# Kernel tuning notes

Measured on AMD Instinct MI355X. Metric: run time of the kernel, lower is better.

## Reference

```python
import jax, jax.numpy as jnp
import numpy as np
from jax.ops import segment_sum, segment_max

N_NODES = 50000
N_GRAPHS = 64
EPS = 1e-16


def gat_layer(x, src, dst, W, a_src, a_dst, b, n_nodes):
    # PyG GATConv, heads=1: shared linear, additive attention, per-dst softmax
    h = x @ W                                  # [N, H]
    al_s = h @ a_src                           # [N]
    al_d = h @ a_dst                           # [N]
    e = jax.nn.leaky_relu(al_s[src] + al_d[dst], 0.2)   # [E]
    # numerically stable segment softmax over edges grouped by dst
    m = segment_max(e, dst, num_segments=n_nodes)
    m = jnp.where(jnp.isfinite(m), m, 0.0)
    ex = jnp.exp(e - m[dst])
    denom = segment_sum(ex, dst, num_segments=n_nodes)
    alpha = ex / (denom[dst] + EPS)            # [E]
    out = segment_sum(alpha[:, None] * h[src], dst, num_segments=n_nodes)
    return out + b


def setup_inputs() -> dict:
    key = jax.random.key(0)
    ks = jax.random.split(key, 16)
    H = 128
    x = jax.random.normal(ks[0], (N_NODES, 4), dtype=jnp.float32)
    edge_index = jax.random.randint(ks[1], (2, 800000), 0, N_NODES, dtype=jnp.int64)
    batch = jnp.sort(jax.random.randint(ks[2], (N_NODES,), 0, N_GRAPHS, dtype=jnp.int64))

    def glorot(k, shape):
        lim = np.sqrt(6.0 / (shape[0] + shape[-1]))
        return jax.random.uniform(k, shape, jnp.float32, -lim, lim)

    params = {
        'W1': glorot(ks[3], (4, H)), 'as1': glorot(ks[4], (H,)), 'ad1': glorot(ks[5], (H,)), 'b1': jnp.zeros((H,), jnp.float32),
        'W2': glorot(ks[6], (H, H)), 'as2': glorot(ks[7], (H,)), 'ad2': glorot(ks[8], (H,)), 'b2': jnp.zeros((H,), jnp.float32),
        'W3': glorot(ks[9], (H, H)), 'as3': glorot(ks[10], (H,)), 'ad3': glorot(ks[11], (H,)), 'b3': jnp.zeros((H,), jnp.float32),
        'Wlin': glorot(ks[12], (H, 2)), 'blin': jnp.zeros((2,), jnp.float32),
    }
    return {'x': x, 'edge_index': edge_index, 'batch': batch, **params}


def reference(x, edge_index, batch, W1, as1, ad1, b1, W2, as2, ad2, b2, W3, as3, ad3, b3, Wlin, blin):
    n = x.shape[0]
    # GATConv default add_self_loops=True
    loop = jnp.arange(n, dtype=edge_index.dtype)
    src = jnp.concatenate([edge_index[0], loop])
    dst = jnp.concatenate([edge_index[1], loop])

    h = jax.nn.relu(gat_layer(x, src, dst, W1, as1, ad1, b1, n))
    h = jax.nn.relu(gat_layer(h, src, dst, W2, as2, ad2, b2, n))
    h = gat_layer(h, src, dst, W3, as3, ad3, b3, n)

    # global_mean_pool
    sums = segment_sum(h, batch, num_segments=N_GRAPHS)          # [G, H]
    cnt = segment_sum(jnp.ones((n,), h.dtype), batch, num_segments=N_GRAPHS)
    pooled = sums / jnp.maximum(cnt, 1.0)[:, None]
    # dropout p=0.5 is identity in eval mode
    return pooled @ Wlin + blin                                   # [G, 2]
```

## Files before the change

kernel.cpp:

```cpp
#include <hip/hip_runtime.h>
#include <math.h>


#define BW 512
#define PART_CHUNK 4096

__device__ __forceinline__ float bflo(unsigned u) { return __uint_as_float(u << 16); }
__device__ __forceinline__ float bfhi(unsigned u) { return __uint_as_float(u & 0xffff0000u); }
__device__ __forceinline__ unsigned pk2bf(float a, float b) {
  unsigned ua = __float_as_uint(a); ua += 0x7fffu + ((ua >> 16) & 1u);
  unsigned ub = __float_as_uint(b); ub += 0x7fffu + ((ub >> 16) & 1u);
  return (ua >> 16) | (ub & 0xffff0000u);
}

__global__ __launch_bounds__(256) void kb_hist(const int* __restrict__ ei,
                                               int* __restrict__ bcnt,
                                               int E, int ET, int NB) {
  __shared__ int h[128];
  int tid = threadIdx.x;
  if (tid < 128) h[tid] = 0;
  __syncthreads();
  int stride = gridDim.x * 256;
  for (int i = blockIdx.x * 256 + tid; i < ET; i += stride) {
    int dst = (i < E) ? ei[E + i] : (i - E);
    atomicAdd(&h[dst >> 9], 1);
  }
  __syncthreads();
  if (tid < NB && h[tid] > 0) atomicAdd(&bcnt[tid], h[tid]);
}

__global__ __launch_bounds__(128) void kb_scan(const int* __restrict__ bcnt,
                                               int* __restrict__ bbase,
                                               int* __restrict__ bcur,
                                               int* __restrict__ rowp,
                                               int N, int ET, int NB) {
  __shared__ int sm[128];
  int t = threadIdx.x;
  int v = (t < NB) ? bcnt[t] : 0;
  sm[t] = v;
  __syncthreads();
  for (int off = 1; off < 128; off <<= 1) {
    int u = (t >= off) ? sm[t - off] : 0;
    __syncthreads();
    sm[t] += u;
    __syncthreads();
  }
  int pre = sm[t] - v;
  if (t <= NB) bbase[t] = pre;
  if (t < NB) bcur[t] = pre;
  if (t == 0) rowp[N] = ET;
}

__global__ __launch_bounds__(256) void kb_part(const int* __restrict__ ei,
                                               int* __restrict__ bcur,
                                               int* __restrict__ bucketed,
                                               int E, int ET, int NB) {
  __shared__ int hist[128];
  __shared__ int runb[128];
  int tid = threadIdx.x;
  int base = blockIdx.x * PART_CHUNK;
  if (tid < 128) hist[tid] = 0;

  int sv[16], dv[16];
#pragma unroll
  for (int k = 0; k < 16; ++k) {
    int j = base + k * 256 + tid;
    int s = -1, d = 0;
    if (j < ET) {
      if (j < E) { s = ei[j]; d = ei[E + j]; }
      else       { s = j - E; d = j - E; }
    }
    sv[k] = s; dv[k] = d;
  }
  __syncthreads();
#pragma unroll
  for (int k = 0; k < 16; ++k)
    if (sv[k] >= 0) atomicAdd(&hist[dv[k] >> 9], 1);
  __syncthreads();
  if (tid < NB && hist[tid] > 0) runb[tid] = atomicAdd(&bcur[tid], hist[tid]);
  __syncthreads();
  if (tid < 128) hist[tid] = 0;
  __syncthreads();
#pragma unroll
  for (int k = 0; k < 16; ++k) {
    if (sv[k] >= 0) {
      int b = dv[k] >> 9;
      int off = atomicAdd(&hist[b], 1);
      bucketed[runb[b] + off] = (sv[k] << 9) | (dv[k] & (BW - 1));
    }
  }
}

__global__ __launch_bounds__(256) void kb_csr(const int* __restrict__ bucketed,
                                              const int* __restrict__ bbase,
                                              int* __restrict__ rowp,
                                              int* __restrict__ csr,
                                              int N) {
  __shared__ int h[512];
  __shared__ int sm[256];
  __shared__ int cur[512];
  int tid = threadIdx.x;
  int b = blockIdx.x;
  int cb = bbase[b], ce = bbase[b + 1];

  h[tid] = 0; h[tid + 256] = 0;
  __syncthreads();
  for (int j = cb + tid; j < ce; j += 256)
    atomicAdd(&h[bucketed[j] & (BW - 1)], 1);
  __syncthreads();
  int a0 = h[2 * tid], a1 = h[2 * tid + 1];
  int s = a0 + a1;
  sm[tid] = s;
  __syncthreads();
  for (int off = 1; off < 256; off <<= 1) {
    int u = (tid >= off) ? sm[tid - off] : 0;
    __syncthreads();
    sm[tid] += u;
    __syncthreads();
  }
  int pre = sm[tid] - s;
  cur[2 * tid] = pre;
  cur[2 * tid + 1] = pre + a0;
  __syncthreads();
  int node0 = b * BW;
  for (int local = tid; local < BW; local += 256) {
    int node = node0 + local;
    if (node < N) rowp[node] = cb + cur[local];
  }
  __syncthreads();
  for (int j = cb + tid; j < ce; j += 256) {
    int p = bucketed[j];
    int loc = p & (BW - 1);
    int pos = cb + atomicAdd(&cur[loc], 1);
    csr[pos] = (unsigned)p >> 9;
  }
}

__global__ __launch_bounds__(256) void k_gemm4al(const float* __restrict__ X,
                                                 const float* __restrict__ W,
                                                 const float* __restrict__ asv,
                                                 const float* __restrict__ adv,
                                                 float* __restrict__ Hout,
                                                 unsigned* __restrict__ Hbf,
                                                 float* __restrict__ al_s,
                                                 float* __restrict__ al_d, int N) {
  int wid = threadIdx.x >> 6, lane = threadIdx.x & 63;
  int node = blockIdx.x * 4 + wid;
  if (node >= N) return;
  float4 xv = *(const float4*)(X + node * 4);
  int f = lane * 2;
  float2 w0 = *(const float2*)(W + f);
  float2 w1 = *(const float2*)(W + 128 + f);
  float2 w2 = *(const float2*)(W + 256 + f);
  float2 w3 = *(const float2*)(W + 384 + f);
  float h0 = xv.x * w0.x + xv.y * w1.x + xv.z * w2.x + xv.w * w3.x;
  float h1 = xv.x * w0.y + xv.y * w1.y + xv.z * w2.y + xv.w * w3.y;
  float2 hv = {h0, h1};
  *(float2*)(Hout + node * 128 + f) = hv;
  Hbf[node * 64 + lane] = pk2bf(h0, h1);
  float2 s2 = *(const float2*)(asv + f);
  float2 d2 = *(const float2*)(adv + f);
  float ps = h0 * s2.x + h1 * s2.y;
  float pd = h0 * d2.x + h1 * d2.y;
  for (int off = 32; off; off >>= 1) {
    ps += __shfl_xor(ps, off);
    pd += __shfl_xor(pd, off);
  }
  if (lane == 0) { al_s[node] = ps; al_d[node] = pd; }
}

__global__ __launch_bounds__(256) void k_gemm128al(const float* __restrict__ X,
                                                   const float* __restrict__ W,
                                                   const float* __restrict__ asv,
                                                   const float* __restrict__ adv,
                                                   float* __restrict__ Hout,
                                                   uint4* __restrict__ Hbf,
                                                   float* __restrict__ al_s,
                                                   float* __restrict__ al_d, int N) {
  __shared__ float Ws[64 * 128];
  __shared__ float Xs[64 * 68];
  int tid = threadIdx.x;
  int base = blockIdx.x * 64;
  int ty = tid >> 4, tx = tid & 15;

  float acc[4][8];
#pragma unroll
  for (int r = 0; r < 4; ++r)
#pragma unroll
    for (int c = 0; c < 8; ++c) acc[r][c] = 0.f;

  for (int kk = 0; kk < 128; kk += 64) {
    __syncthreads();
    for (int i = tid * 4; i < 64 * 128; i += 1024) {
      *(float4*)(Ws + i) = *(const float4*)(W + kk * 128 + i);
    }
    for (int i = tid; i < 64 * 16; i += 256) {
      int node = i >> 4, k4 = (i & 15) << 2;
      int gn = base + node;
      float4 v;
      if (gn < N) v = *(const float4*)(X + gn * 128 + kk + k4);
      else        v = make_float4(0.f, 0.f, 0.f, 0.f);
      *(float4*)(Xs + node * 68 + k4) = v;
    }
    __syncthreads();

    for (int k = 0; k < 64; ++k) {
      float a0 = Xs[(ty * 4 + 0) * 68 + k];
      float a1 = Xs[(ty * 4 + 1) * 68 + k];
      float a2 = Xs[(ty * 4 + 2) * 68 + k];
      float a3 = Xs[(ty * 4 + 3) * 68 + k];
      float4 b0 = *(const float4*)(Ws + k * 128 + tx * 8);
      float4 b1 = *(const float4*)(Ws + k * 128 + tx * 8 + 4);
      acc[0][0] += a0 * b0.x; acc[0][1] += a0 * b0.y; acc[0][2] += a0 * b0.z; acc[0][3] += a0 * b0.w;
      acc[0][4] += a0 * b1.x; acc[0][5] += a0 * b1.y; acc[0][6] += a0 * b1.z; acc[0][7] += a0 * b1.w;
      acc[1][0] += a1 * b0.x; acc[1][1] += a1 * b0.y; acc[1][2] += a1 * b0.z; acc[1][3] += a1 * b0.w;
      acc[1][4] += a1 * b1.x; acc[1][5] += a1 * b1.y; acc[1][6] += a1 * b1.z; acc[1][7] += a1 * b1.w;
      acc[2][0] += a2 * b0.x; acc[2][1] += a2 * b0.y; acc[2][2] += a2 * b0.z; acc[2][3] += a2 * b0.w;
      acc[2][4] += a2 * b1.x; acc[2][5] += a2 * b1.y; acc[2][6] += a2 * b1.z; acc[2][7] += a2 * b1.w;
      acc[3][0] += a3 * b0.x; acc[3][1] += a3 * b0.y; acc[3][2] += a3 * b0.z; acc[3][3] += a3 * b0.w;
      acc[3][4] += a3 * b1.x; acc[3][5] += a3 * b1.y; acc[3][6] += a3 * b1.z; acc[3][7] += a3 * b1.w;
    }
  }

  float4 as0 = *(const float4*)(asv + tx * 8);
  float4 as1 = *(const float4*)(asv + tx * 8 + 4);
  float4 ad0 = *(const float4*)(adv + tx * 8);
  float4 ad1 = *(const float4*)(adv + tx * 8 + 4);
#pragma unroll
  for (int r = 0; r < 4; ++r) {
    int gn = base + ty * 4 + r;
    float ps = acc[r][0] * as0.x + acc[r][1] * as0.y + acc[r][2] * as0.z + acc[r][3] * as0.w
             + acc[r][4] * as1.x + acc[r][5] * as1.y + acc[r][6] * as1.z + acc[r][7] * as1.w;
    float pd = acc[r][0] * ad0.x + acc[r][1] * ad0.y + acc[r][2] * ad0.z + acc[r][3] * ad0.w
             + acc[r][4] * ad1.x + acc[r][5] * ad1.y + acc[r][6] * ad1.z + acc[r][7] * ad1.w;
    for (int off = 1; off < 16; off <<= 1) {
      ps += __shfl_xor(ps, off);
      pd += __shfl_xor(pd, off);
    }
    if (gn < N) {
      float4 o0 = make_float4(acc[r][0], acc[r][1], acc[r][2], acc[r][3]);
      float4 o1 = make_float4(acc[r][4], acc[r][5], acc[r][6], acc[r][7]);
      *(float4*)(Hout + gn * 128 + tx * 8) = o0;
      *(float4*)(Hout + gn * 128 + tx * 8 + 4) = o1;
      uint4 pb;
      pb.x = pk2bf(acc[r][0], acc[r][1]);
      pb.y = pk2bf(acc[r][2], acc[r][3]);
      pb.z = pk2bf(acc[r][4], acc[r][5]);
      pb.w = pk2bf(acc[r][6], acc[r][7]);
      Hbf[(size_t)gn * 16 + tx] = pb;
      if (tx == 0) { al_s[gn] = ps; al_d[gn] = pd; }
    }
  }
}

__global__ __launch_bounds__(256) void k_agg(const int* __restrict__ csr_src,
                                             const int* __restrict__ rowp,
                                             const float* __restrict__ al_s,
                                             const float* __restrict__ al_d,
                                             const float* __restrict__ Hh,
                                             const uint4* __restrict__ Hbf,
                                             const float* __restrict__ bias,
                                             float* __restrict__ exw,
                                             float* __restrict__ Yout, int N, int relu) {
  int wid = threadIdx.x >> 6, lane = threadIdx.x & 63;
  int dst = blockIdx.x * 4 + wid;
  if (dst >= N) return;
  int beg = rowp[dst], end = rowp[dst + 1];
  int deg = end - beg;
  float ald = al_d[dst];

  int q = lane >> 4;
  int l = lane & 15;
  float acc[8];
#pragma unroll
  for (int c = 0; c < 8; ++c) acc[c] = 0.f;

  if (deg <= 64) {
    int srcv = 0;
    float e = -INFINITY;
    if (lane < deg) {
      srcv = csr_src[beg + lane];
      e = al_s[srcv] + ald;
      e = (e > 0.f) ? e : 0.2f * e;
    }
    float m = e;
    for (int off = 32; off; off >>= 1) m = fmaxf(m, __shfl_xor(m, off));
    float av = (lane < deg) ? __expf(e - m) : 0.f;
    float den = av;
    for (int off = 32; off; off >>= 1) den += __shfl_xor(den, off);
    av *= 1.0f / (den + 1e-16f);

    int t = 0;
    for (; t + 8 <= deg; t += 8) {
      int sA = __shfl(srcv, t + q);
      int sB = __shfl(srcv, t + 4 + q);
      float wA = __shfl(av, t + q);
      float wB = __shfl(av, t + 4 + q);
      uint4 va = Hbf[(size_t)sA * 16 + l];
      uint4 vb = Hbf[(size_t)sB * 16 + l];
      acc[0] += wA * bflo(va.x) + wB * bflo(vb.x);
      acc[1] += wA * bfhi(va.x) + wB * bfhi(vb.x);
      acc[2] += wA * bflo(va.y) + wB * bflo(vb.y);
      acc[3] += wA * bfhi(va.y) + wB * bfhi(vb.y);
      acc[4] += wA * bflo(va.z) + wB * bflo(vb.z);
      acc[5] += wA * bfhi(va.z) + wB * bfhi(vb.z);
      acc[6] += wA * bflo(va.w) + wB * bflo(vb.w);
      acc[7] += wA * bfhi(va.w) + wB * bfhi(vb.w);
    }
    if (t + 4 <= deg) {
      int sA = __shfl(srcv, t + q);
      float wA = __shfl(av, t + q);
      uint4 va = Hbf[(size_t)sA * 16 + l];
      acc[0] += wA * bflo(va.x); acc[1] += wA * bfhi(va.x);
      acc[2] += wA * bflo(va.y); acc[3] += wA * bfhi(va.y);
      acc[4] += wA * bflo(va.z); acc[5] += wA * bfhi(va.z);
      acc[6] += wA * bflo(va.w); acc[7] += wA * bfhi(va.w);
      t += 4;
    }
    {
      int sA = __shfl(srcv, t + q);
      float wA = __shfl(av, t + q);
      if (t + q < deg) {
        uint4 va = Hbf[(size_t)sA * 16 + l];
        acc[0] += wA * bflo(va.x); acc[1] += wA * bfhi(va.x);
        acc[2] += wA * bflo(va.y); acc[3] += wA * bfhi(va.y);
        acc[4] += wA * bflo(va.z); acc[5] += wA * bfhi(va.z);
        acc[6] += wA * bflo(va.w); acc[7] += wA * bfhi(va.w);
      }
    }
  } else {
    const float* Hl = Hh + l * 8;
    float m = -INFINITY;
    for (int j = beg + lane; j < end; j += 64) {
      float e = al_s[csr_src[j]] + ald;
      e = (e > 0.f) ? e : 0.2f * e;
      exw[j] = e;
      m = fmaxf(m, e);
    }
    for (int off = 32; off; off >>= 1) m = fmaxf(m, __shfl_xor(m, off));

    float den = 0.f;
    for (int j = beg + lane; j < end; j += 64) {
      float ex = __expf(exw[j] - m);
      exw[j] = ex;
      den += ex;
    }
    for (int off = 32; off; off >>= 1) den += __shfl_xor(den, off);
    float inv = 1.0f / (den + 1e-16f);

    int j = beg;
    for (; j + 8 <= end; j += 8) {
      int sA = csr_src[j + q];
      int sB = csr_src[j + 4 + q];
      float wA = exw[j + q] * inv;
      float wB = exw[j + 4 + q] * inv;
      const float* rA = Hl + (size_t)sA * 128;
      const float* rB = Hl + (size_t)sB * 128;
      float4 a0 = *(const float4*)(rA);
      float4 a1 = *(const float4*)(rA + 4);
      float4 b0 = *(const float4*)(rB);
      float4 b1 = *(const float4*)(rB + 4);
      acc[0] += wA * a0.x + wB * b0.x;
      acc[1] += wA * a0.y + wB * b0.y;
      acc[2] += wA * a0.z + wB * b0.z;
      acc[3] += wA * a0.w + wB * b0.w;
      acc[4] += wA * a1.x + wB * b1.x;
      acc[5] += wA * a1.y + wB * b1.y;
      acc[6] += wA * a1.z + wB * b1.z;
      acc[7] += wA * a1.w + wB * b1.w;
    }
    if (j + 4 <= end) {
      int sA = csr_src[j + q];
      float wA = exw[j + q] * inv;
      const float* rA = Hl + (size_t)sA * 128;
      float4 a0 = *(const float4*)(rA);
      float4 a1 = *(const float4*)(rA + 4);
      acc[0] += wA * a0.x; acc[1] += wA * a0.y; acc[2] += wA * a0.z; acc[3] += wA * a0.w;
      acc[4] += wA * a1.x; acc[5] += wA * a1.y; acc[6] += wA * a1.z; acc[7] += wA * a1.w;
      j += 4;
    }
    if (j + q < end) {
      int sA = csr_src[j + q];
      float wA = exw[j + q] * inv;
      const float* rA = Hl + (size_t)sA * 128;
      float4 a0 = *(const float4*)(rA);
      float4 a1 = *(const float4*)(rA + 4);
      acc[0] += wA * a0.x; acc[1] += wA * a0.y; acc[2] += wA * a0.z; acc[3] += wA * a0.w;
      acc[4] += wA * a1.x; acc[5] += wA * a1.y; acc[6] += wA * a1.z; acc[7] += wA * a1.w;
    }
  }

#pragma unroll
  for (int c = 0; c < 8; ++c) {
    acc[c] += __shfl_xor(acc[c], 16);
    acc[c] += __shfl_xor(acc[c], 32);
  }
  if (q == 0) {
    float4 bv0 = *(const float4*)(bias + l * 8);
    float4 bv1 = *(const float4*)(bias + l * 8 + 4);
    float4 o0 = make_float4(acc[0] + bv0.x, acc[1] + bv0.y, acc[2] + bv0.z, acc[3] + bv0.w);
    float4 o1 = make_float4(acc[4] + bv1.x, acc[5] + bv1.y, acc[6] + bv1.z, acc[7] + bv1.w);
    if (relu) {
      o0.x = fmaxf(o0.x, 0.f); o0.y = fmaxf(o0.y, 0.f); o0.z = fmaxf(o0.z, 0.f); o0.w = fmaxf(o0.w, 0.f);
      o1.x = fmaxf(o1.x, 0.f); o1.y = fmaxf(o1.y, 0.f); o1.z = fmaxf(o1.z, 0.f); o1.w = fmaxf(o1.w, 0.f);
    }
    *(float4*)(Yout + (size_t)dst * 128 + l * 8) = o0;
    *(float4*)(Yout + (size_t)dst * 128 + l * 8 + 4) = o1;
  }
}

__global__ __launch_bounds__(256) void k_pool(const float* __restrict__ Hh,
                                              const int* __restrict__ batch,
                                              float* __restrict__ gsum,
                                              float* __restrict__ gcnt,
                                              int N, int nwaves) {
  int gw = (blockIdx.x * 256 + threadIdx.x) >> 6;
  int lane = threadIdx.x & 63;
  int chunk = (N + nwaves - 1) / nwaves;
  int beg = gw * chunk;
  int end = beg + chunk; if (end > N) end = N;
  if (beg >= end) return;

  int curg = batch[beg];
  float2 acc = {0.f, 0.f};
  int cnt = 0;
  for (int n = beg; n < end; ++n) {
    int g = batch[n];
    if (g != curg) {
      atomicAdd(&gsum[curg * 128 + lane * 2], acc.x);
      atomicAdd(&gsum[curg * 128 + lane * 2 + 1], acc.y);
      if (lane == 0) atomicAdd(&gcnt[curg], (float)cnt);
      acc.x = 0.f; acc.y = 0.f; cnt = 0; curg = g;
    }
    float2 h = *(const float2*)(Hh + (size_t)n * 128 + lane * 2);
    acc.x += h.x; acc.y += h.y; ++cnt;
  }
  atomicAdd(&gsum[curg * 128 + lane * 2], acc.x);
  atomicAdd(&gsum[curg * 128 + lane * 2 + 1], acc.y);
  if (lane == 0) atomicAdd(&gcnt[curg], (float)cnt);
}

__global__ __launch_bounds__(128) void k_final(const float* __restrict__ gsum,
                                               const float* __restrict__ gcnt,
                                               const float* __restrict__ Wlin,
                                               const float* __restrict__ blin,
                                               float* __restrict__ out) {
  int t = threadIdx.x;
  int g = t >> 1, c = t & 1;
  float inv = 1.0f / fmaxf(gcnt[g], 1.0f);
  float acc = blin[c];
  for (int k = 0; k < 128; ++k) acc += gsum[g * 128 + k] * inv * Wlin[k * 2 + c];
  out[g * 2 + c] = acc;
}

extern "C" void kernel_launch(void* const* d_in, const int* in_sizes, int n_in,
                              void* d_out, int out_size, void* d_ws, size_t ws_size,
                              hipStream_t stream) {
  const float* x    = (const float*)d_in[0];
  const int*   ei   = (const int*)d_in[1];
  const int*   batch= (const int*)d_in[2];
  const float* W1   = (const float*)d_in[3];
  const float* as1  = (const float*)d_in[4];
  const float* ad1  = (const float*)d_in[5];
  const float* b1   = (const float*)d_in[6];
  const float* W2   = (const float*)d_in[7];
  const float* as2  = (const float*)d_in[8];
  const float* ad2  = (const float*)d_in[9];
  const float* b2   = (const float*)d_in[10];
  const float* W3   = (const float*)d_in[11];
  const float* as3  = (const float*)d_in[12];
  const float* ad3  = (const float*)d_in[13];
  const float* b3   = (const float*)d_in[14];
  const float* Wlin = (const float*)d_in[15];
  const float* blin = (const float*)d_in[16];

  int N = in_sizes[0] / 4;
  int E = in_sizes[1] / 2;
  int ET = E + N;
  int NB = (N + BW - 1) / BW;

  char* ws = (char*)d_ws;
  float* bufA = (float*)ws; ws += (size_t)N * 128 * 4;
  float* bufB = (float*)ws; ws += (size_t)N * 128 * 4;
  unsigned* hbf = (unsigned*)ws; ws += (size_t)N * 128 * 2;
  float* al_s = (float*)ws; ws += (size_t)N * 4;
  float* al_d = (float*)ws; ws += (size_t)N * 4;
  float* gsum = (float*)ws; ws += (size_t)64 * 128 * 4;
  float* gcnt = (float*)ws; ws += (size_t)64 * 4;
  int* rowp   = (int*)ws;   ws += (size_t)(N + 1) * 4;
  int* csr    = (int*)ws;   ws += (size_t)ET * 4;
  float* exw  = (float*)ws; ws += (size_t)ET * 4;
  int* bucketed = (int*)ws; ws += (size_t)ET * 4;
  int* bcnt   = (int*)ws;   ws += (size_t)128 * 4;
  int* bbase  = (int*)ws;   ws += (size_t)132 * 4;
  int* bcur   = (int*)ws;   ws += (size_t)128 * 4;

  hipMemsetAsync(bcnt, 0, (size_t)128 * 4, stream);
  hipMemsetAsync(gsum, 0, (size_t)(64 * 128 + 64) * 4, stream);

  kb_hist<<<256, 256, 0, stream>>>(ei, bcnt, E, ET, NB);
  kb_scan<<<1, 128, 0, stream>>>(bcnt, bbase, bcur, rowp, N, ET, NB);
  kb_part<<<(ET + PART_CHUNK - 1) / PART_CHUNK, 256, 0, stream>>>(ei, bcur, bucketed, E, ET, NB);
  kb_csr <<<NB, 256, 0, stream>>>(bucketed, bbase, rowp, csr, N);

  int nb4 = (N + 3) / 4;
  k_gemm4al<<<nb4, 256, 0, stream>>>(x, W1, as1, ad1, bufA, hbf, al_s, al_d, N);
  k_agg    <<<nb4, 256, 0, stream>>>(csr, rowp, al_s, al_d, bufA, (const uint4*)hbf, b1, exw, bufB, N, 1);
  k_gemm128al<<<(N + 63) / 64, 256, 0, stream>>>(bufB, W2, as2, ad2, bufA, (uint4*)hbf, al_s, al_d, N);
  k_agg      <<<nb4, 256, 0, stream>>>(csr, rowp, al_s, al_d, bufA, (const uint4*)hbf, b2, exw, bufB, N, 1);
  k_gemm128al<<<(N + 63) / 64, 256, 0, stream>>>(bufB, W3, as3, ad3, bufA, (uint4*)hbf, al_s, al_d, N);
  k_agg      <<<nb4, 256, 0, stream>>>(csr, rowp, al_s, al_d, bufA, (const uint4*)hbf, b3, exw, bufB, N, 0);

  k_pool <<<256, 256, 0, stream>>>(bufB, batch, gsum, gcnt, N, 1024);
  k_final<<<1, 128, 0, stream>>>(gsum, gcnt, Wlin, blin, (float*)d_out);
}
```

Baseline: 368.9 us.

## Use bf16 MFMA for hidden GEMMs and keep activations in bf16

Replaces the fp32 SIMT 128x128 GEMM with a bf16 MFMA kernel (16x16x32) fed by a pre-transposed bf16 copy of W2/W3 built in a new prep kernel. Aggregation now writes bf16 activations for the relu layers and gathers bf16 neighbor rows in the large-degree path, and the fp32 H copies are no longer written. This cuts GEMM compute time and memory traffic on the intermediate buffers, at the cost of extra bf16 rounding on GEMM inputs and weights, which loosens accuracy.

```diff
diff --git a/kernel.cpp b/kernel.cpp
--- a/kernel.cpp
+++ b/kernel.cpp
@@ -4,6 +4,9 @@
 
 #define BW 512
 #define PART_CHUNK 4096
+
+typedef __attribute__((ext_vector_type(8))) short short8v;
+typedef __attribute__((ext_vector_type(4))) float f32x4;
 
 __device__ __forceinline__ float bflo(unsigned u) { return __uint_as_float(u << 16); }
 __device__ __forceinline__ float bfhi(unsigned u) { return __uint_as_float(u & 0xffff0000u); }
@@ -136,11 +139,24 @@
   }
 }
 
+__global__ __launch_bounds__(256) void k_prep(const float* __restrict__ W2,
+                                              const float* __restrict__ W3,
+                                              unsigned short* __restrict__ Wcm2,
+                                              unsigned short* __restrict__ Wcm3) {
+  int i = blockIdx.x * 256 + threadIdx.x;
+  if (i < 16384) {
+    int k = i >> 7, n = i & 127;
+    unsigned u = __float_as_uint(W2[i]); u += 0x7fffu + ((u >> 16) & 1u);
+    Wcm2[n * 128 + k] = (unsigned short)(u >> 16);
+    unsigned v = __float_as_uint(W3[i]); v += 0x7fffu + ((v >> 16) & 1u);
+    Wcm3[n * 128 + k] = (unsigned short)(v >> 16);
+  }
+}
+
 __global__ __launch_bounds__(256) void k_gemm4al(const float* __restrict__ X,
                                                  const float* __restrict__ W,
                                                  const float* __restrict__ asv,
                                                  const float* __restrict__ adv,
-                                                 float* __restrict__ Hout,
                                                  unsigned* __restrict__ Hbf,
                                                  float* __restrict__ al_s,
                                                  float* __restrict__ al_d, int N) {
@@ -155,8 +171,6 @@
   float2 w3 = *(const float2*)(W + 384 + f);
   float h0 = xv.x * w0.x + xv.y * w1.x + xv.z * w2.x + xv.w * w3.x;
   float h1 = xv.x * w0.y + xv.y * w1.y + xv.z * w2.y + xv.w * w3.y;
-  float2 hv = {h0, h1};
-  *(float2*)(Hout + node * 128 + f) = hv;
   Hbf[node * 64 + lane] = pk2bf(h0, h1);
   float2 s2 = *(const float2*)(asv + f);
   float2 d2 = *(const float2*)(adv + f);
@@ -169,86 +183,67 @@
   if (lane == 0) { al_s[node] = ps; al_d[node] = pd; }
 }
 
-__global__ __launch_bounds__(256) void k_gemm128al(const float* __restrict__ X,
-                                                   const float* __restrict__ W,
-                                                   const float* __restrict__ asv,
-                                                   const float* __restrict__ adv,
-                                                   float* __restrict__ Hout,
-                                                   uint4* __restrict__ Hbf,
-                                                   float* __restrict__ al_s,
-                                                   float* __restrict__ al_d, int N) {
-  __shared__ float Ws[64 * 128];
-  __shared__ float Xs[64 * 68];
-  int tid = threadIdx.x;
-  int base = blockIdx.x * 64;
-  int ty = tid >> 4, tx = tid & 15;
-
-  float acc[4][8];
-#pragma unroll
-  for (int r = 0; r < 4; ++r)
-#pragma unroll
-    for (int c = 0; c < 8; ++c) acc[r][c] = 0.f;
-
-  for (int kk = 0; kk < 128; kk += 64) {
-    __syncthreads();
-    for (int i = tid * 4; i < 64 * 128; i += 1024) {
-      *(float4*)(Ws + i) = *(const float4*)(W + kk * 128 + i);
-    }
-    for (int i = tid; i < 64 * 16; i += 256) {
-      int node = i >> 4, k4 = (i & 15) << 2;
-      int gn = base + node;
-      float4 v;
-      if (gn < N) v = *(const float4*)(X + gn * 128 + kk + k4);
-      else        v = make_float4(0.f, 0.f, 0.f, 0.f);
-      *(float4*)(Xs + node * 68 + k4) = v;
-    }
-    __syncthreads();
-
-    for (int k = 0; k < 64; ++k) {
-      float a0 = Xs[(ty * 4 + 0) * 68 + k];
-      float a1 = Xs[(ty * 4 + 1) * 68 + k];
-      float a2 = Xs[(ty * 4 + 2) * 68 + k];
-      float a3 = Xs[(ty * 4 + 3) * 68 + k];
-      float4 b0 = *(const float4*)(Ws + k * 128 + tx * 8);
-      float4 b1 = *(const float4*)(Ws + k * 128 + tx * 8 + 4);
-      acc[0][0] += a0 * b0.x; acc[0][1] += a0 * b0.y; acc[0][2] += a0 * b0.z; acc[0][3] += a0 * b0.w;
-      acc[0][4] += a0 * b1.x; acc[0][5] += a0 * b1.y; acc[0][6] += a0 * b1.z; acc[0][7] += a0 * b1.w;
-      acc[1][0] += a1 * b0.x; acc[1][1] += a1 * b0.y; acc[1][2] += a1 * b0.z; acc[1][3] += a1 * b0.w;
-      acc[1][4] += a1 * b1.x; acc[1][5] += a1 * b1.y; acc[1][6] += a1 * b1.z; acc[1][7] += a1 * b1.w;
-      acc[2][0] += a2 * b0.x; acc[2][1] += a2 * b0.y; acc[2][2] += a2 * b0.z; acc[2][3] += a2 * b0.w;
-      acc[2][4] += a2 * b1.x; acc[2][5] += a2 * b1.y; acc[2][6] += a2 * b1.z; acc[2][7] += a2 * b1.w;
-      acc[3][0] += a3 * b0.x; acc[3][1] += a3 * b0.y; acc[3][2] += a3 * b0.z; acc[3][3] += a3 * b0.w;
-      acc[3][4] += a3 * b1.x; acc[3][5] += a3 * b1.y; acc[3][6] += a3 * b1.z; acc[3][7] += a3 * b1.w;
-    }
-  }
-
-  float4 as0 = *(const float4*)(asv + tx * 8);
-  float4 as1 = *(const float4*)(asv + tx * 8 + 4);
-  float4 ad0 = *(const float4*)(adv + tx * 8);
-  float4 ad1 = *(const float4*)(adv + tx * 8 + 4);
-#pragma unroll
-  for (int r = 0; r < 4; ++r) {
-    int gn = base + ty * 4 + r;
-    float ps = acc[r][0] * as0.x + acc[r][1] * as0.y + acc[r][2] * as0.z + acc[r][3] * as0.w
-             + acc[r][4] * as1.x + acc[r][5] * as1.y + acc[r][6] * as1.z + acc[r][7] * as1.w;
-    float pd = acc[r][0] * ad0.x + acc[r][1] * ad0.y + acc[r][2] * ad0.z + acc[r][3] * ad0.w
-             + acc[r][4] * ad1.x + acc[r][5] * ad1.y + acc[r][6] * ad1.z + acc[r][7] * ad1.w;
+__global__ __launch_bounds__(256) void k_gemm128mfma(
+    const unsigned short* __restrict__ Xbf,
+    const unsigned short* __restrict__ Wcm,
+    const float* __restrict__ asv, const float* __restrict__ adv,
+    unsigned* __restrict__ Hbf,
+    float* __restrict__ al_s, float* __restrict__ al_d, int N) {
+  int wid = threadIdx.x >> 6, lane = threadIdx.x & 63;
+  int c = lane & 15, g = lane >> 4;
+  int row0 = blockIdx.x * 64 + wid * 16;
+  int arow = row0 + c;
+  int arowc = (arow < N) ? arow : (N - 1);
+
+  short8v a[4];
+#pragma unroll
+  for (int kt = 0; kt < 4; ++kt)
+    a[kt] = *(const short8v*)(Xbf + (size_t)arowc * 128 + kt * 32 + g * 8);
+
+  f32x4 acc[8];
+#pragma unroll
+  for (int f = 0; f < 8; ++f) acc[f] = (f32x4){0.f, 0.f, 0.f, 0.f};
+
+#pragma unroll
+  for (int f = 0; f < 8; ++f) {
+    const unsigned short* wb = Wcm + (size_t)(f * 16 + c) * 128 + g * 8;
+#pragma unroll
+    for (int kt = 0; kt < 4; ++kt) {
+      short8v b = *(const short8v*)(wb + kt * 32);
+      acc[f] = __builtin_amdgcn_mfma_f32_16x16x32_bf16(a[kt], b, acc[f], 0, 0, 0);
+    }
+  }
+
+  float ps[4] = {0.f, 0.f, 0.f, 0.f}, pd[4] = {0.f, 0.f, 0.f, 0.f};
+#pragma unroll
+  for (int f = 0; f < 8; ++f) {
+    float as_c = asv[f * 16 + c], ad_c = adv[f * 16 + c];
+#pragma unroll
+    for (int j = 0; j < 4; ++j) { ps[j] += acc[f][j] * as_c; pd[j] += acc[f][j] * ad_c; }
+  }
+#pragma unroll
+  for (int j = 0; j < 4; ++j) {
     for (int off = 1; off < 16; off <<= 1) {
-      ps += __shfl_xor(ps, off);
-      pd += __shfl_xor(pd, off);
-    }
-    if (gn < N) {
-      float4 o0 = make_float4(acc[r][0], acc[r][1], acc[r][2], acc[r][3]);
-      float4 o1 = make_float4(acc[r][4], acc[r][5], acc[r][6], acc[r][7]);
-      *(float4*)(Hout + gn * 128 + tx * 8) = o0;
-      *(float4*)(Hout + gn * 128 + tx * 8 + 4) = o1;
-      uint4 pb;
-      pb.x = pk2bf(acc[r][0], acc[r][1]);
-      pb.y = pk2bf(acc[r][2], acc[r][3]);
-      pb.z = pk2bf(acc[r][4], acc[r][5]);
-      pb.w = pk2bf(acc[r][6], acc[r][7]);
-      Hbf[(size_t)gn * 16 + tx] = pb;
-      if (tx == 0) { al_s[gn] = ps; al_d[gn] = pd; }
+      ps[j] += __shfl_xor(ps[j], off);
+      pd[j] += __shfl_xor(pd[j], off);
+    }
+  }
+  if (c == 0) {
+#pragma unroll
+    for (int j = 0; j < 4; ++j) {
+      int r = row0 + g * 4 + j;
+      if (r < N) { al_s[r] = ps[j]; al_d[r] = pd[j]; }
+    }
+  }
+
+#pragma unroll
+  for (int f = 0; f < 8; ++f) {
+#pragma unroll
+    for (int j = 0; j < 4; ++j) {
+      float partner = __shfl_xor(acc[f][j], 1);
+      int r = row0 + g * 4 + j;
+      if (((lane & 1) == 0) && r < N)
+        Hbf[(size_t)r * 64 + f * 8 + (c >> 1)] = pk2bf(acc[f][j], partner);
     }
   }
 }
@@ -257,11 +252,12 @@
                                              const int* __restrict__ rowp,
                                              const float* __restrict__ al_s,
                                              const float* __restrict__ al_d,
-                                             const float* __restrict__ Hh,
                                              const uint4* __restrict__ Hbf,
                                              const float* __restrict__ bias,
                                              float* __restrict__ exw,
-                                             float* __restrict__ Yout, int N, int relu) {
+                                             float* __restrict__ Yf32,
+                                             uint4* __restrict__ Ybf,
+                                             int N, int relu) {
   int wid = threadIdx.x >> 6, lane = threadIdx.x & 63;
   int dst = blockIdx.x * 4 + wid;
   if (dst >= N) return;
@@ -329,7 +325,6 @@
       }
     }
   } else {
-    const float* Hl = Hh + l * 8;
     float m = -INFINITY;
     for (int j = beg + lane; j < end; j += 64) {
       float e = al_s[csr_src[j]] + ald;
@@ -348,45 +343,14 @@
     for (int off = 32; off; off >>= 1) den += __shfl_xor(den, off);
     float inv = 1.0f / (den + 1e-16f);
 
-    int j = beg;
-    for (; j + 8 <= end; j += 8) {
-      int sA = csr_src[j + q];
-      int sB = csr_src[j + 4 + q];
-      float wA = exw[j + q] * inv;
-      float wB = exw[j + 4 + q] * inv;
-      const float* rA = Hl + (size_t)sA * 128;
-      const float* rB = Hl + (size_t)sB * 128;
-      float4 a0 = *(const float4*)(rA);
-      float4 a1 = *(const float4*)(rA + 4);
-      float4 b0 = *(const float4*)(rB);
-      float4 b1 = *(const float4*)(rB + 4);
-      acc[0] += wA * a0.x + wB * b0.x;
-      acc[1] += wA * a0.y + wB * b0.y;
-      acc[2] += wA * a0.z + wB * b0.z;
-      acc[3] += wA * a0.w + wB * b0.w;
-      acc[4] += wA * a1.x + wB * b1.x;
-      acc[5] += wA * a1.y + wB * b1.y;
-      acc[6] += wA * a1.z + wB * b1.z;
-      acc[7] += wA * a1.w + wB * b1.w;
-    }
-    if (j + 4 <= end) {
-      int sA = csr_src[j + q];
-      float wA = exw[j + q] * inv;
-      const float* rA = Hl + (size_t)sA * 128;
-      float4 a0 = *(const float4*)(rA);
-      float4 a1 = *(const float4*)(rA + 4);
-      acc[0] += wA * a0.x; acc[1] += wA * a0.y; acc[2] += wA * a0.z; acc[3] += wA * a0.w;
-      acc[4] += wA * a1.x; acc[5] += wA * a1.y; acc[6] += wA * a1.z; acc[7] += wA * a1.w;
-      j += 4;
-    }
-    if (j + q < end) {
-      int sA = csr_src[j + q];
-      float wA = exw[j + q] * inv;
-      const float* rA = Hl + (size_t)sA * 128;
-      float4 a0 = *(const float4*)(rA);
-      float4 a1 = *(const float4*)(rA + 4);
-      acc[0] += wA * a0.x; acc[1] += wA * a0.y; acc[2] += wA * a0.z; acc[3] += wA * a0.w;
-      acc[4] += wA * a1.x; acc[5] += wA * a1.y; acc[6] += wA * a1.z; acc[7] += wA * a1.w;
+    for (int j = beg + q; j < end; j += 4) {
+      int sA = csr_src[j];
+      float wA = exw[j] * inv;
+      uint4 va = Hbf[(size_t)sA * 16 + l];
+      acc[0] += wA * bflo(va.x); acc[1] += wA * bfhi(va.x);
+      acc[2] += wA * bflo(va.y); acc[3] += wA * bfhi(va.y);
+      acc[4] += wA * bflo(va.z); acc[5] += wA * bfhi(va.z);
+      acc[6] += wA * bflo(va.w); acc[7] += wA * bfhi(va.w);
     }
   }
 
@@ -398,14 +362,21 @@
   if (q == 0) {
     float4 bv0 = *(const float4*)(bias + l * 8);
     float4 bv1 = *(const float4*)(bias + l * 8 + 4);
-    float4 o0 = make_float4(acc[0] + bv0.x, acc[1] + bv0.y, acc[2] + bv0.z, acc[3] + bv0.w);
-    float4 o1 = make_float4(acc[4] + bv1.x, acc[5] + bv1.y, acc[6] + bv1.z, acc[7] + bv1.w);
+    float o0 = acc[0] + bv0.x, o1 = acc[1] + bv0.y, o2 = acc[2] + bv0.z, o3 = acc[3] + bv0.w;
+    float o4 = acc[4] + bv1.x, o5 = acc[5] + bv1.y, o6 = acc[6] + bv1.z, o7 = acc[7] + bv1.w;
     if (relu) {
-      o0.x = fmaxf(o0.x, 0.f); o0.y = fmaxf(o0.y, 0.f); o0.z = fmaxf(o0.z, 0.f); o0.w = fmaxf(o0.w, 0.f);
-      o1.x = fmaxf(o1.x, 0.f); o1.y = fmaxf(o1.y, 0.f); o1.z = fmaxf(o1.z, 0.f); o1.w = fmaxf(o1.w, 0.f);
-    }
-    *(float4*)(Yout + (size_t)dst * 128 + l * 8) = o0;
-    *(float4*)(Yout + (size_t)dst * 128 + l * 8 + 4) = o1;
+      o0 = fmaxf(o0, 0.f); o1 = fmaxf(o1, 0.f); o2 = fmaxf(o2, 0.f); o3 = fmaxf(o3, 0.f);
+      o4 = fmaxf(o4, 0.f); o5 = fmaxf(o5, 0.f); o6 = fmaxf(o6, 0.f); o7 = fmaxf(o7, 0.f);
+      uint4 pb;
+      pb.x = pk2bf(o0, o1); pb.y = pk2bf(o2, o3);
+      pb.z = pk2bf(o4, o5); pb.w = pk2bf(o6, o7);
+      Ybf[(size_t)dst * 16 + l] = pb;
+    } else {
+      float4 w0 = make_float4(o0, o1, o2, o3);
+      float4 w1 = make_float4(o4, o5, o6, o7);
+      *(float4*)(Yf32 + (size_t)dst * 128 + l * 8) = w0;
+      *(float4*)(Yf32 + (size_t)dst * 128 + l * 8 + 4) = w1;
+    }
   }
 }
 
@@ -480,9 +451,9 @@
   int NB = (N + BW - 1) / BW;
 
   char* ws = (char*)d_ws;
-  float* bufA = (float*)ws; ws += (size_t)N * 128 * 4;
-  float* bufB = (float*)ws; ws += (size_t)N * 128 * 4;
-  unsigned* hbf = (unsigned*)ws; ws += (size_t)N * 128 * 2;
+  unsigned* bfA = (unsigned*)ws; ws += (size_t)N * 64 * 4;
+  unsigned* bfB = (unsigned*)ws; ws += (size_t)N * 64 * 4;
+  float* bufY = (float*)ws; ws += (size_t)N * 128 * 4;
   float* al_s = (float*)ws; ws += (size_t)N * 4;
   float* al_d = (float*)ws; ws += (size_t)N * 4;
   float* gsum = (float*)ws; ws += (size_t)64 * 128 * 4;
@@ -494,6 +465,8 @@
   int* bcnt   = (int*)ws;   ws += (size_t)128 * 4;
   int* bbase  = (int*)ws;   ws += (size_t)132 * 4;
   int* bcur   = (int*)ws;   ws += (size_t)128 * 4;
+  unsigned short* wcm2 = (unsigned short*)ws; ws += (size_t)128 * 128 * 2;
+  unsigned short* wcm3 = (unsigned short*)ws; ws += (size_t)128 * 128 * 2;
 
   hipMemsetAsync(bcnt, 0, (size_t)128 * 4, stream);
   hipMemsetAsync(gsum, 0, (size_t)(64 * 128 + 64) * 4, stream);
@@ -502,15 +475,17 @@
   kb_scan<<<1, 128, 0, stream>>>(bcnt, bbase, bcur, rowp, N, ET, NB);
   kb_part<<<(ET + PART_CHUNK - 1) / PART_CHUNK, 256, 0, stream>>>(ei, bcur, bucketed, E, ET, NB);
   kb_csr <<<NB, 256, 0, stream>>>(bucketed, bbase, rowp, csr, N);
+  k_prep <<<64, 256, 0, stream>>>(W2, W3, wcm2, wcm3);
 
   int nb4 = (N + 3) / 4;
-  k_gemm4al<<<nb4, 256, 0, stream>>>(x, W1, as1, ad1, bufA, hbf, al_s, al_d, N);
-  k_agg    <<<nb4, 256, 0, stream>>>(csr, rowp, al_s, al_d, bufA, (const uint4*)hbf, b1, exw, bufB, N, 1);
-  k_gemm128al<<<(N + 63) / 64, 256, 0, stream>>>(bufB, W2, as2, ad2, bufA, (uint4*)hbf, al_s, al_d, N);
-  k_agg      <<<nb4, 256, 0, stream>>>(csr, rowp, al_s, al_d, bufA, (const uint4*)hbf, b2, exw, bufB, N, 1);
-  k_gemm128al<<<(N + 63) / 64, 256, 0, stream>>>(bufB, W3, as3, ad3, bufA, (uint4*)hbf, al_s, al_d, N);
-  k_agg      <<<nb4, 256, 0, stream>>>(csr, rowp, al_s, al_d, bufA, (const uint4*)hbf, b3, exw, bufB, N, 0);
-
-  k_pool <<<256, 256, 0, stream>>>(bufB, batch, gsum, gcnt, N, 1024);
+  int nb64 = (N + 63) / 64;
+  k_gemm4al<<<nb4, 256, 0, stream>>>(x, W1, as1, ad1, bfA, al_s, al_d, N);
+  k_agg    <<<nb4, 256, 0, stream>>>(csr, rowp, al_s, al_d, (const uint4*)bfA, b1, exw, bufY, (uint4*)bfB, N, 1);
+  k_gemm128mfma<<<nb64, 256, 0, stream>>>((const unsigned short*)bfB, wcm2, as2, ad2, bfA, al_s, al_d, N);
+  k_agg        <<<nb4, 256, 0, stream>>>(csr, rowp, al_s, al_d, (const uint4*)bfA, b2, exw, bufY, (uint4*)bfB, N, 1);
+  k_gemm128mfma<<<nb64, 256, 0, stream>>>((const unsigned short*)bfB, wcm3, as3, ad3, bfA, al_s, al_d, N);
+  k_agg        <<<nb4, 256, 0, stream>>>(csr, rowp, al_s, al_d, (const uint4*)bfA, b3, exw, bufY, (uint4*)bfB, N, 0);
+
+  k_pool <<<256, 256, 0, stream>>>(bufY, batch, gsum, gcnt, N, 1024);
   k_final<<<1, 128, 0, stream>>>(gsum, gcnt, Wlin, blin, (float*)d_out);
 }
```

Result: faster. 346.9 us (-6.0%).
